# Kernel optimization log

Measured on AMD Instinct MI355X. Metric: run time of the kernel, lower is better.

## Reference

```python
import jax, jax.numpy as jnp
import numpy as np

B, T, C, H = 2, 2048, 1024, 16
HS = C // H  # head_size = 64
EPS = 1e-5


def _ln(x, g, b):
    m = jnp.mean(x, axis=-1, keepdims=True)
    v = jnp.mean(jnp.square(x - m), axis=-1, keepdims=True)
    return (x - m) * jax.lax.rsqrt(v + EPS) * g + b


def setup_inputs() -> dict:
    key = jax.random.key(0)
    ks = jax.random.split(key, 16)
    s = lambda k, shape, fan: jax.random.normal(k, shape, jnp.float32) * (fan ** -0.5)
    return {
        "x": jax.random.normal(ks[0], (B, T, C), jnp.float32),
        "Wq": s(ks[1], (H, C, HS), C), "bq": jnp.zeros((H, HS), jnp.float32),
        "Wk": s(ks[2], (H, C, HS), C), "bk": jnp.zeros((H, HS), jnp.float32),
        "Wv": s(ks[3], (H, C, HS), C), "bv": jnp.zeros((H, HS), jnp.float32),
        "Wo": s(ks[4], (C, C), C), "bo": jnp.zeros((C,), jnp.float32),
        "g1": jnp.ones((C,), jnp.float32), "b1": jnp.zeros((C,), jnp.float32),
        "g2": jnp.ones((C,), jnp.float32), "b2": jnp.zeros((C,), jnp.float32),
        "W1": s(ks[5], (C, C), C), "bf1": jnp.zeros((C,), jnp.float32),
        "W2": s(ks[6], (C, C), C), "bf2": jnp.zeros((C,), jnp.float32),
    }


def _block(x, Wq, bq, Wk, bk, Wv, bv, Wo, bo, g1, b1, g2, b2, W1, bf1, W2, bf2):
    h = _ln(x, g1, b1)
    # per-head projections, batched over heads: (B,T,C) x (H,C,HS) -> (B,H,T,HS)
    q = jnp.einsum('btc,hcd->bhtd', h, Wq) + bq[None, :, None, :]
    k = jnp.einsum('btc,hcd->bhtd', h, Wk) + bk[None, :, None, :]
    v = jnp.einsum('btc,hcd->bhtd', h, Wv) + bv[None, :, None, :]
    w = jnp.einsum('bhqd,bhkd->bhqk', q, k) * (HS ** -0.5)
    causal = jnp.tril(jnp.ones((T, T), bool))  # tril[q,k]==0 -> -inf
    w = jnp.where(causal[None, None], w, -jnp.inf)
    # FAITHFUL quirk: original uses F.softmax(w, dim=1) on (B,T,T),
    # i.e. normalization over the QUERY axis (axis=2 of bhqk).
    w = jax.nn.softmax(w, axis=2)
    att = jnp.einsum('bhqk,bhkd->bhqd', w, v)
    att = att.transpose(0, 2, 1, 3).reshape(x.shape[0], x.shape[1], -1)  # concat heads
    x = x + att @ Wo + bo
    h2 = _ln(x, g2, b2)
    x = x + jax.nn.relu(h2 @ W1 + bf1) @ W2 + bf2
    return x


def reference(x, Wq, bq, Wk, bk, Wv, bv, Wo, bo, g1, b1, g2, b2, W1, bf1, W2, bf2):
    return _block(x, Wq, bq, Wk, bk, Wv, bv, Wo, bo, g1, b1, g2, b2, W1, bf1, W2, bf2)
```

## Files before the change

### kernel.cpp

```cpp
#include <hip/hip_runtime.h>
#include <hip/hip_bf16.h>
#include <math.h>


#define B_   2
#define T_   2048
#define C_   1024
#define H_   16
#define HS_  64
#define NROWS 4096
#define C3   3072
#define K1C  0.1803368801111244f

typedef unsigned short ushort_t;
typedef __attribute__((ext_vector_type(8))) short short8;
typedef __attribute__((ext_vector_type(4))) float f32x4;
typedef __attribute__((ext_vector_type(16))) float f32x16;

__device__ __forceinline__ ushort_t f2bf(float f) {
  __hip_bfloat16 h = __float2bfloat16(f);
  ushort_t u; __builtin_memcpy(&u, &h, 2); return u;
}
__device__ __forceinline__ float bf2f(ushort_t u) {
  union { unsigned u; float f; } v; v.u = ((unsigned)u) << 16;
  return v.f;
}
__device__ __forceinline__ unsigned pkhw(float a, float b) {
  unsigned u;
  asm("v_cvt_pk_bf16_f32 %0, %1, %2" : "=v"(u) : "v"(a), "v"(b));
  return u;
}
__device__ __forceinline__ short8 mk8(unsigned a, unsigned b, unsigned c, unsigned d) {
  union { unsigned u[4]; short8 s; } t;
  t.u[0] = a; t.u[1] = b; t.u[2] = c; t.u[3] = d; return t.s;
}
__device__ __forceinline__ void pl32swap(unsigned &a, unsigned &b) {
  asm("v_permlane32_swap_b32 %0, %1" : "+v"(a), "+v"(b));
}
__device__ __forceinline__ f32x4 mfma16(short8 a, short8 b, f32x4 c) {
  return __builtin_amdgcn_mfma_f32_16x16x32_bf16(a, b, c, 0, 0, 0);
}
__device__ __forceinline__ f32x16 mfma32(short8 a, short8 b, f32x16 c) {
  return __builtin_amdgcn_mfma_f32_32x32x16_bf16(a, b, c, 0, 0, 0);
}
typedef const __attribute__((address_space(1))) void g_void;
typedef __attribute__((address_space(3))) void l_void;
__device__ __forceinline__ void gl_lds16(const void* g, void* l) {
  __builtin_amdgcn_global_load_lds((g_void*)g, (l_void*)l, 16, 0, 0);
}

__global__ __launch_bounds__(256) void ln_bf16(
    const float* __restrict__ x, const float* __restrict__ g,
    const float* __restrict__ b, ushort_t* __restrict__ out) {
  int row = blockIdx.x;
  const float* xr = x + (size_t)row * C_;
  int t = threadIdx.x;
  float4 v = ((const float4*)xr)[t];
  float s  = v.x + v.y + v.z + v.w;
  float ss = v.x*v.x + v.y*v.y + v.z*v.z + v.w*v.w;
  #pragma unroll
  for (int off = 32; off > 0; off >>= 1) {
    s  += __shfl_down(s, off);
    ss += __shfl_down(ss, off);
  }
  __shared__ float red[2][4];
  int wid = t >> 6, lane = t & 63;
  if (lane == 0) { red[0][wid] = s; red[1][wid] = ss; }
  __syncthreads();
  if (t == 0) {
    float a = 0, c = 0;
    for (int i = 0; i < 4; i++) { a += red[0][i]; c += red[1][i]; }
    red[0][0] = a; red[1][0] = c;
  }
  __syncthreads();
  float mean = red[0][0] * (1.0f / C_);
  float var  = red[1][0] * (1.0f / C_) - mean * mean;
  float r = rsqrtf(var + 1e-5f);
  float4 gv = ((const float4*)g)[t];
  float4 bv = ((const float4*)b)[t];
  ushort4 o;
  o.x = f2bf((v.x - mean) * r * gv.x + bv.x);
  o.y = f2bf((v.y - mean) * r * gv.y + bv.y);
  o.z = f2bf((v.z - mean) * r * gv.z + bv.z);
  o.w = f2bf((v.w - mean) * r * gv.w + bv.w);
  ((ushort4*)(out + (size_t)row * C_))[t] = o;
}

__global__ __launch_bounds__(256) void prep_weights(
    const float* __restrict__ Wq, const float* __restrict__ Wk,
    const float* __restrict__ Wv, const float* __restrict__ Wo,
    const float* __restrict__ W1, const float* __restrict__ W2,
    const float* __restrict__ bq, const float* __restrict__ bk,
    const float* __restrict__ bv, ushort_t* __restrict__ Wqkvt,
    ushort_t* __restrict__ Wot3, float* __restrict__ bqkv) {
  int bid = blockIdx.x;
  if (bid < 12288) {
    int idx = bid * 256 + threadIdx.x;
    int n = idx >> 10, c = idx & 1023;
    int sel = n >> 10, nn = n & 1023;
    const float* W = (sel == 0) ? Wq : ((sel == 1) ? Wk : Wv);
    Wqkvt[idx] = f2bf(W[((size_t)(nn >> 6) * C_ + c) * HS_ + (nn & 63)]);
  } else if (bid < 24576) {
    int idx = (bid - 12288) * 256 + threadIdx.x;
    int sel = idx >> 20, rem = idx & 1048575;
    int n = rem >> 10, k = rem & 1023;
    const float* W = (sel == 0) ? Wo : ((sel == 1) ? W1 : W2);
    Wot3[idx] = f2bf(W[(size_t)k * C_ + n]);
  } else {
    int i = (bid - 24576) * 256 + threadIdx.x;
    if (i < 3072)
      bqkv[i] = (i < 1024) ? bq[i] : ((i < 2048) ? bk[i - 1024] : bv[i - 2048]);
  }
}

__global__ __launch_bounds__(256) void gemm128q(
    const ushort_t* __restrict__ A, const ushort_t* __restrict__ Bt,
    const float* __restrict__ bias, ushort_t* __restrict__ Cm,
    int M, int N, int K) {
  __shared__ ushort_t As[128 * 64];
  __shared__ ushort_t Bs[128 * 64];
  int t = threadIdx.x;
  int bid = blockIdx.x;
  int xcd = bid & 7, loc = bid >> 3;
  int mb = (xcd >> 1) * 8 + (loc & 7);
  int nb = (xcd & 1) * 12 + (loc >> 3);
  int m0 = mb * 128, n0 = nb * 128;
  int w = t >> 6, l = t & 63;
  int wr = w >> 1, wc = w & 1;
  int lo = l & 15, hi = l >> 4;
  f32x4 acc[4][4] = {};
  int srow = t >> 3, ssw = (t & 7) ^ (srow & 7);
  const ushort_t* Ag = A  + (size_t)(m0 + srow) * K + ssw * 8;
  const ushort_t* Bg = Bt + (size_t)(n0 + srow) * K + ssw * 8;
  int aoff[4][2], boff[4][2];
  #pragma unroll
  for (int i = 0; i < 4; i++)
    #pragma unroll
    for (int kk = 0; kk < 2; kk++) {
      aoff[i][kk] = (wr * 64 + i * 16 + lo) * 64 + ((kk * 4 + hi) ^ (lo & 7)) * 8;
      boff[i][kk] = (wc * 64 + i * 16 + lo) * 64 + ((kk * 4 + hi) ^ (lo & 7)) * 8;
    }
  for (int k0 = 0; k0 < K; k0 += 64) {
    #pragma unroll
    for (int i = 0; i < 4; i++) {
      gl_lds16(Ag + (size_t)(i * 32) * K + k0, &As[i * 2048 + t * 8]);
      gl_lds16(Bg + (size_t)(i * 32) * K + k0, &Bs[i * 2048 + t * 8]);
    }
    __syncthreads();
    short8 af[4][2], bfr[4][2];
    #pragma unroll
    for (int i = 0; i < 4; i++)
      #pragma unroll
      for (int kk = 0; kk < 2; kk++) {
        af[i][kk]  = *(const short8*)&As[aoff[i][kk]];
        bfr[i][kk] = *(const short8*)&Bs[boff[i][kk]];
      }
    #pragma unroll
    for (int kk = 0; kk < 2; kk++)
      #pragma unroll
      for (int i = 0; i < 4; i++)
        #pragma unroll
        for (int j = 0; j < 4; j++)
          acc[i][j] = mfma16(af[i][kk], bfr[j][kk], acc[i][j]);
    __syncthreads();
  }
  float qs = (n0 < C_) ? K1C : 1.0f;
  #pragma unroll
  for (int i = 0; i < 4; i++) {
    int m = m0 + wr * 64 + i * 16 + hi * 4;
    #pragma unroll
    for (int j = 0; j < 4; j++) {
      int n = n0 + wc * 64 + j * 16 + lo;
      float bv = bias[n];
      #pragma unroll
      for (int r = 0; r < 4; r++)
        Cm[(size_t)(m + r) * N + n] = f2bf((acc[i][j][r] + bv) * qs);
    }
  }
}

template<int OUT_BF16, int RELU, int HAS_RES>
__global__ __launch_bounds__(256) void gemm64(
    const ushort_t* __restrict__ A, const ushort_t* __restrict__ Bt,
    const float* __restrict__ bias, const float* __restrict__ res,
    void* __restrict__ Cm, int M, int N, int K) {
  __shared__ ushort_t As[128 * 64];
  __shared__ ushort_t Bs[64 * 64];
  int t = threadIdx.x;
  int m0 = blockIdx.y * 128, n0 = blockIdx.x * 64;
  int w = t >> 6, l = t & 63;
  int wr = w >> 1, wc = w & 1;
  int lo = l & 15, hi = l >> 4;
  f32x4 acc[4][2] = {};
  int srow = t >> 3, ssw = (t & 7) ^ (srow & 7);
  const ushort_t* Ag = A  + (size_t)(m0 + srow) * K + ssw * 8;
  const ushort_t* Bg = Bt + (size_t)(n0 + srow) * K + ssw * 8;
  int aoff[4][2], boff[2][2];
  #pragma unroll
  for (int i = 0; i < 4; i++)
    #pragma unroll
    for (int kk = 0; kk < 2; kk++)
      aoff[i][kk] = (wr * 64 + i * 16 + lo) * 64 + ((kk * 4 + hi) ^ (lo & 7)) * 8;
  #pragma unroll
  for (int j = 0; j < 2; j++)
    #pragma unroll
    for (int kk = 0; kk < 2; kk++)
      boff[j][kk] = (wc * 32 + j * 16 + lo) * 64 + ((kk * 4 + hi) ^ (lo & 7)) * 8;
  for (int k0 = 0; k0 < K; k0 += 64) {
    #pragma unroll
    for (int i = 0; i < 4; i++)
      gl_lds16(Ag + (size_t)(i * 32) * K + k0, &As[i * 2048 + t * 8]);
    #pragma unroll
    for (int i = 0; i < 2; i++)
      gl_lds16(Bg + (size_t)(i * 32) * K + k0, &Bs[i * 2048 + t * 8]);
    __syncthreads();
    short8 af[4][2], bfr[2][2];
    #pragma unroll
    for (int i = 0; i < 4; i++)
      #pragma unroll
      for (int kk = 0; kk < 2; kk++)
        af[i][kk] = *(const short8*)&As[aoff[i][kk]];
    #pragma unroll
    for (int j = 0; j < 2; j++)
      #pragma unroll
      for (int kk = 0; kk < 2; kk++)
        bfr[j][kk] = *(const short8*)&Bs[boff[j][kk]];
    #pragma unroll
    for (int kk = 0; kk < 2; kk++)
      #pragma unroll
      for (int i = 0; i < 4; i++)
        #pragma unroll
        for (int j = 0; j < 2; j++)
          acc[i][j] = mfma16(af[i][kk], bfr[j][kk], acc[i][j]);
    __syncthreads();
  }
  #pragma unroll
  for (int i = 0; i < 4; i++) {
    int m = m0 + wr * 64 + i * 16 + hi * 4;
    #pragma unroll
    for (int j = 0; j < 2; j++) {
      int n = n0 + wc * 32 + j * 16 + lo;
      float bv = bias[n];
      #pragma unroll
      for (int r = 0; r < 4; r++) {
        float v = acc[i][j][r] + bv;
        if (HAS_RES) v += res[(size_t)(m + r) * N + n];
        if (RELU) v = fmaxf(v, 0.f);
        if (OUT_BF16) ((ushort_t*)Cm)[(size_t)(m + r) * N + n] = f2bf(v);
        else          ((float*)Cm)[(size_t)(m + r) * N + n] = v;
      }
    }
  }
}

__global__ __launch_bounds__(256) void attn_stats(
    const ushort_t* __restrict__ QKV, float* __restrict__ dinv) {
  int bid = blockIdx.x;
  int xcd = bid & 7, loc = (bid >> 3) & 31, half = bid >> 8;
  int bh = xcd * 4 + (loc & 3);
  int j = loc >> 2;
  int kb = half ? (15 - j) : j;
  int b = bh >> 4, h = bh & 15;
  int t = threadIdx.x, w = t >> 6, l = t & 63, l31 = l & 31, hi32 = l >> 5;
  __shared__ ushort_t Qs[2][4][2048];
  const ushort_t* Qb = QKV + (size_t)b * T_ * C3 + h * HS_;
  const ushort_t* Kb = Qb + C_;
  int k0w = kb * 128 + w * 32;
  short8 ka[4];
  #pragma unroll
  for (int c = 0; c < 4; c++)
    ka[c] = *(const short8*)(Kb + (size_t)(k0w + l31) * C3 + c * 16 + hi32 * 8);
  float s[16];
  #pragma unroll
  for (int r = 0; r < 16; r++) s[r] = 0.f;

  int qoff[4];
  #pragma unroll
  for (int c = 0; c < 4; c++)
    qoff[c] = l31 * 64 + ((c * 2 + hi32) ^ (l31 & 7)) * 8;

  int sr = t >> 3, slot = t & 7, su = slot ^ (sr & 7);
  const ushort_t* Qsrc = Qb + (size_t)sr * C3 + su * 8;
  int qt0 = kb * 4, cnt = 64 - qt0;
  int dqt = qt0 + w;

  #pragma unroll
  for (int sub = 0; sub < 4; sub++)
    gl_lds16(Qsrc + (size_t)(qt0 + sub) * 32 * C3, &Qs[0][sub][t * 8]);
  for (int i = 0; i < cnt; i += 4) {
    int buf = (i >> 2) & 1;
    if (i + 4 < cnt) {
      #pragma unroll
      for (int sub = 0; sub < 4; sub++)
        gl_lds16(Qsrc + (size_t)(qt0 + i + 4 + sub) * 32 * C3,
                 &Qs[buf ^ 1][sub][t * 8]);
      asm volatile("s_waitcnt vmcnt(4)");
    } else {
      asm volatile("s_waitcnt vmcnt(0)");
    }
    __builtin_amdgcn_s_barrier();
    __builtin_amdgcn_sched_barrier(0);
    #pragma unroll
    for (int sub = 0; sub < 4; sub++) {
      int qt = qt0 + i + sub;
      if (qt >= dqt) {
        const ushort_t* base = &Qs[buf][sub][0];
        short8 qf[4];
        #pragma unroll
        for (int c = 0; c < 4; c++)
          qf[c] = *(const short8*)(base + qoff[c]);
        __builtin_amdgcn_s_setprio(1);
        f32x16 d = {};
        #pragma unroll
        for (int c = 0; c < 4; c++) d = mfma32(ka[c], qf[c], d);
        __builtin_amdgcn_s_setprio(0);
        if (qt == dqt) {
          int qq = qt * 32 + l31;
          #pragma unroll
          for (int r = 0; r < 16; r++) {
            int k = k0w + (r & 3) + 8 * (r >> 2) + 4 * hi32;
            s[r] += (qq >= k) ? __builtin_amdgcn_exp2f(d[r]) : 0.f;
          }
        } else {
          #pragma unroll
          for (int r = 0; r < 16; r++) s[r] += __builtin_amdgcn_exp2f(d[r]);
        }
      }
    }
    __builtin_amdgcn_sched_barrier(0);
    __builtin_amdgcn_s_barrier();
    __builtin_amdgcn_sched_barrier(0);
  }
  #pragma unroll
  for (int off = 1; off < 32; off <<= 1)
    #pragma unroll
    for (int r = 0; r < 16; r++)
      s[r] += __shfl_xor(s[r], off);
  if (l31 == 0) {
    #pragma unroll
    for (int r = 0; r < 16; r++) {
      int k = k0w + (r & 3) + 8 * (r >> 2) + 4 * hi32;
      dinv[(size_t)bh * T_ + k] = 1.0f / s[r];
    }
  }
}

__global__ __launch_bounds__(256) void transpose_v(
    const ushort_t* __restrict__ QKV, const float* __restrict__ dinv,
    ushort_t* __restrict__ Vt) {
  int t0 = blockIdx.x * 64;
  int bh = blockIdx.y; int b = bh >> 4, h = bh & 15;
  __shared__ ushort_t tile[64][65];
  int tid = threadIdx.x;
  #pragma unroll
  for (int i = 0; i < 16; i++) {
    int idx = i * 256 + tid;
    int tt = idx >> 6, dd = idx & 63;
    float v = bf2f(QKV[(size_t)(b * T_ + t0 + tt) * C3 + 2 * C_ + h * HS_ + dd]);
    tile[tt][dd] = f2bf(v * dinv[(size_t)bh * T_ + t0 + tt]);
  }
  __syncthreads();
  #pragma unroll
  for (int i = 0; i < 16; i++) {
    int idx = i * 256 + tid;
    int dd = idx >> 6, tt = idx & 63;
    Vt[((size_t)(bh * HS_ + dd)) * T_ + t0 + tt] = tile[tt][dd];
  }
}

__global__ __launch_bounds__(256) void attn_pv(
    const ushort_t* __restrict__ QKV, const ushort_t* __restrict__ Vt,
    ushort_t* __restrict__ att) {
  int bid = blockIdx.x;
  int xcd = bid & 7, loc = (bid >> 3) & 31, half = bid >> 8;
  int bh = xcd * 4 + (loc & 3);
  int j = loc >> 2;
  int qb = half ? j : (15 - j);
  int b = bh >> 4, h = bh & 15;
  int t = threadIdx.x, w = t >> 6, l = t & 63, l31 = l & 31, hi32 = l >> 5;
  __shared__ ushort_t KV[2][4][2][2048];
  const ushort_t* Qb = QKV + (size_t)b * T_ * C3 + h * HS_;
  const ushort_t* Kb = Qb + C_;
  const ushort_t* Vb = Vt + (size_t)bh * HS_ * T_;
  int q0w = qb * 128 + w * 32;
  short8 qf[4];
  #pragma unroll
  for (int c = 0; c < 4; c++)
    qf[c] = *(const short8*)(Qb + (size_t)(q0w + l31) * C3 + c * 16 + hi32 * 8);
  f32x16 o0 = {}, o1 = {};
  int nkt = qb * 4 + 4;
  int dkt = q0w >> 5;

  int koff[4], voff[4];
  #pragma unroll
  for (int c = 0; c < 4; c++)
    koff[c] = l31 * 64 + ((c * 2 + hi32) ^ (l31 & 7)) * 8;
  #pragma unroll
  for (int i = 0; i < 4; i++) {
    int u = (i & 1) * 4 + (i >> 1) * 2 + hi32;
    voff[i] = 2048 + l31 * 64 + (u ^ (l31 & 7)) * 8;
  }

  int sr = t >> 3, slot = t & 7, su = slot ^ (sr & 7);
  int vdh = su >> 2, vc2 = su & 3;
  const ushort_t* Ksrc = Kb + (size_t)sr * C3 + su * 8;
  const ushort_t* Vsrc = Vb + (size_t)(vdh * 32 + sr) * T_ + vc2 * 8;

  #pragma unroll
  for (int sub = 0; sub < 4; sub++) {
    gl_lds16(Ksrc + (size_t)sub * 32 * C3, &KV[0][sub][0][t * 8]);
    gl_lds16(Vsrc + sub * 32,              &KV[0][sub][1][t * 8]);
  }
  for (int kt = 0; kt < nkt; kt += 4) {
    int buf = (kt >> 2) & 1;
    if (kt + 4 < nkt) {
      #pragma unroll
      for (int sub = 0; sub < 4; sub++) {
        gl_lds16(Ksrc + (size_t)(kt + 4 + sub) * 32 * C3, &KV[buf ^ 1][sub][0][t * 8]);
        gl_lds16(Vsrc + (kt + 4 + sub) * 32,              &KV[buf ^ 1][sub][1][t * 8]);
      }
      asm volatile("s_waitcnt vmcnt(8)");
    } else {
      asm volatile("s_waitcnt vmcnt(0)");
    }
    __builtin_amdgcn_s_barrier();
    __builtin_amdgcn_sched_barrier(0);
    #pragma unroll
    for (int sub = 0; sub < 4; sub++) {
      int kts = kt + sub;
      if (kts <= dkt) {
        const ushort_t* base = &KV[buf][sub][0][0];
        short8 ka[4], vf[4];
        #pragma unroll
        for (int c = 0; c < 4; c++)
          ka[c] = *(const short8*)(base + koff[c]);
        #pragma unroll
        for (int i = 0; i < 4; i++)
          vf[i] = *(const short8*)(base + voff[i]);
        __builtin_amdgcn_s_setprio(1);
        f32x16 sacc = {};
        #pragma unroll
        for (int c = 0; c < 4; c++) sacc = mfma32(ka[c], qf[c], sacc);
        __builtin_amdgcn_s_setprio(0);
        float e[16];
        if (kts == dkt) {
          int qq = q0w + l31;
          #pragma unroll
          for (int r = 0; r < 16; r++) {
            int k = kts * 32 + (r & 3) + 8 * (r >> 2) + 4 * hi32;
            e[r] = (k <= qq) ? __builtin_amdgcn_exp2f(sacc[r]) : 0.f;
          }
        } else {
          #pragma unroll
          for (int r = 0; r < 16; r++) e[r] = __builtin_amdgcn_exp2f(sacc[r]);
        }
        unsigned u[8];
        #pragma unroll
        for (int j2 = 0; j2 < 8; j2++) u[j2] = pkhw(e[2 * j2], e[2 * j2 + 1]);
        pl32swap(u[0], u[2]); pl32swap(u[1], u[3]);
        pl32swap(u[4], u[6]); pl32swap(u[5], u[7]);
        short8 pa0 = mk8(u[0], u[1], u[2], u[3]);
        short8 pa1 = mk8(u[4], u[5], u[6], u[7]);
        __builtin_amdgcn_s_setprio(1);
        o0 = mfma32(pa0, vf[0], o0);
        o1 = mfma32(pa0, vf[1], o1);
        o0 = mfma32(pa1, vf[2], o0);
        o1 = mfma32(pa1, vf[3], o1);
        __builtin_amdgcn_s_setprio(0);
      }
    }
    __builtin_amdgcn_sched_barrier(0);
    __builtin_amdgcn_s_barrier();
    __builtin_amdgcn_sched_barrier(0);
  }

  #pragma unroll
  for (int r = 0; r < 16; r++) {
    int qq = q0w + (r & 3) + 8 * (r >> 2) + 4 * hi32;
    size_t base = (size_t)(b * T_ + qq) * C_ + h * HS_;
    att[base + l31]      = f2bf(o0[r]);
    att[base + 32 + l31] = f2bf(o1[r]);
  }
}

extern "C" void kernel_launch(void* const* d_in, const int* in_sizes, int n_in,
                              void* d_out, int out_size, void* d_ws, size_t ws_size,
                              hipStream_t stream) {
  const float* x   = (const float*)d_in[0];
  const float* Wq  = (const float*)d_in[1];
  const float* bq  = (const float*)d_in[2];
  const float* Wk  = (const float*)d_in[3];
  const float* bk  = (const float*)d_in[4];
  const float* Wv  = (const float*)d_in[5];
  const float* bv  = (const float*)d_in[6];
  const float* Wo  = (const float*)d_in[7];
  const float* bo  = (const float*)d_in[8];
  const float* g1  = (const float*)d_in[9];
  const float* b1  = (const float*)d_in[10];
  const float* g2  = (const float*)d_in[11];
  const float* b2  = (const float*)d_in[12];
  const float* W1  = (const float*)d_in[13];
  const float* bf1 = (const float*)d_in[14];
  const float* W2  = (const float*)d_in[15];
  const float* bf2 = (const float*)d_in[16];
  float* out = (float*)d_out;

  char* base = (char*)d_ws;
  const size_t MB = 1 << 20;
  ushort_t* QKVb  = (ushort_t*)(base);
  ushort_t* hb    = (ushort_t*)(base + 24 * MB);
  ushort_t* Vt    = (ushort_t*)(base + 32 * MB);
  float*    y     = (float*)   (base + 40 * MB);
  ushort_t* Wqkvt = (ushort_t*)(base + 56 * MB);
  ushort_t* Wot   = (ushort_t*)(base + 62 * MB);
  ushort_t* W1t   = (ushort_t*)(base + 64 * MB);
  ushort_t* W2t   = (ushort_t*)(base + 66 * MB);
  float*    bqkv  = (float*)   (base + 68 * MB);
  float*    dinv  = (float*)   (base + 68 * MB + 65536);

  prep_weights<<<24588, 256, 0, stream>>>(Wq, Wk, Wv, Wo, W1, W2,
                                          bq, bk, bv, Wqkvt, Wot, bqkv);

  ln_bf16<<<NROWS, 256, 0, stream>>>(x, g1, b1, hb);

  gemm128q<<<768, 256, 0, stream>>>(hb, Wqkvt, bqkv, QKVb, NROWS, C3, C_);

  attn_stats<<<512, 256, 0, stream>>>(QKVb, dinv);
  transpose_v<<<dim3(T_ / 64, 32), 256, 0, stream>>>(QKVb, dinv, Vt);
  ushort_t* attb = hb;
  attn_pv<<<512, 256, 0, stream>>>(QKVb, Vt, attb);

  dim3 g64(C_ / 64, NROWS / 128);
  gemm64<0,0,1><<<g64, 256, 0, stream>>>(attb, Wot, bo, x, y, NROWS, C_, C_);

  ushort_t* h2b = QKVb;
  ln_bf16<<<NROWS, 256, 0, stream>>>(y, g2, b2, h2b);
  ushort_t* f1b = Vt;
  gemm64<1,1,0><<<g64, 256, 0, stream>>>(h2b, W1t, bf1, nullptr, f1b, NROWS, C_, C_);
  gemm64<0,0,1><<<g64, 256, 0, stream>>>(f1b, W2t, bf2, y, out, NROWS, C_, C_);
}
```

Before: 204.4 us.

## Double-buffer LDS in both GEMM kernels with BK=32 and async prefetch

Both GEMM kernels now use two LDS buffers with K-tiles of 32 instead of one buffer with K-tiles of 64. The next tile's global-to-LDS loads are issued before computing on the current tile, using explicit vmcnt waits and raw barriers, so load latency can overlap with MFMA work. The LDS swizzle is redone for 32-wide rows, and the MFMA section is wrapped in s_setprio. Halving BK doubles the barrier count per unit of work and leaves a shallow prefetch depth.

```diff
diff --git a/kernel.cpp b/kernel.cpp
--- a/kernel.cpp
+++ b/kernel.cpp
@@ -117,8 +117,8 @@
     const ushort_t* __restrict__ A, const ushort_t* __restrict__ Bt,
     const float* __restrict__ bias, ushort_t* __restrict__ Cm,
     int M, int N, int K) {
-  __shared__ ushort_t As[128 * 64];
-  __shared__ ushort_t Bs[128 * 64];
+  __shared__ ushort_t As[2][128 * 32];
+  __shared__ ushort_t Bs[2][128 * 32];
   int t = threadIdx.x;
   int bid = blockIdx.x;
   int xcd = bid & 7, loc = bid >> 3;
@@ -129,40 +129,52 @@
   int wr = w >> 1, wc = w & 1;
   int lo = l & 15, hi = l >> 4;
   f32x4 acc[4][4] = {};
-  int srow = t >> 3, ssw = (t & 7) ^ (srow & 7);
-  const ushort_t* Ag = A  + (size_t)(m0 + srow) * K + ssw * 8;
-  const ushort_t* Bg = Bt + (size_t)(n0 + srow) * K + ssw * 8;
-  int aoff[4][2], boff[4][2];
-  #pragma unroll
-  for (int i = 0; i < 4; i++)
-    #pragma unroll
-    for (int kk = 0; kk < 2; kk++) {
-      aoff[i][kk] = (wr * 64 + i * 16 + lo) * 64 + ((kk * 4 + hi) ^ (lo & 7)) * 8;
-      boff[i][kk] = (wc * 64 + i * 16 + lo) * 64 + ((kk * 4 + hi) ^ (lo & 7)) * 8;
-    }
-  for (int k0 = 0; k0 < K; k0 += 64) {
+  int srow = t >> 2;
+  int sslot = (t & 3) ^ ((srow >> 1) & 3);
+  const ushort_t* Ag = A  + (size_t)(m0 + srow) * K + sslot * 8;
+  const ushort_t* Bg = Bt + (size_t)(n0 + srow) * K + sslot * 8;
+  int key = (lo >> 1) & 3;
+  int aoff[4], boff[4];
+  #pragma unroll
+  for (int i = 0; i < 4; i++) {
+    aoff[i] = (wr * 64 + i * 16 + lo) * 32 + (hi ^ key) * 8;
+    boff[i] = (wc * 64 + i * 16 + lo) * 32 + (hi ^ key) * 8;
+  }
+  int nkt = K >> 5;
+  gl_lds16(Ag,          &As[0][t * 8]);
+  gl_lds16(Ag + 64 * K, &As[0][64 * 32 + t * 8]);
+  gl_lds16(Bg,          &Bs[0][t * 8]);
+  gl_lds16(Bg + 64 * K, &Bs[0][64 * 32 + t * 8]);
+  for (int kt = 0; kt < nkt; kt++) {
+    int cur = kt & 1;
+    if (kt + 1 < nkt) {
+      int k0 = (kt + 1) * 32;
+      gl_lds16(Ag + k0,          &As[cur ^ 1][t * 8]);
+      gl_lds16(Ag + 64 * K + k0, &As[cur ^ 1][64 * 32 + t * 8]);
+      gl_lds16(Bg + k0,          &Bs[cur ^ 1][t * 8]);
+      gl_lds16(Bg + 64 * K + k0, &Bs[cur ^ 1][64 * 32 + t * 8]);
+      asm volatile("s_waitcnt vmcnt(4)");
+    } else {
+      asm volatile("s_waitcnt vmcnt(0)");
+    }
+    __builtin_amdgcn_s_barrier();
+    __builtin_amdgcn_sched_barrier(0);
+    short8 af[4], bfr[4];
     #pragma unroll
     for (int i = 0; i < 4; i++) {
-      gl_lds16(Ag + (size_t)(i * 32) * K + k0, &As[i * 2048 + t * 8]);
-      gl_lds16(Bg + (size_t)(i * 32) * K + k0, &Bs[i * 2048 + t * 8]);
-    }
-    __syncthreads();
-    short8 af[4][2], bfr[4][2];
+      af[i]  = *(const short8*)&As[cur][aoff[i]];
+      bfr[i] = *(const short8*)&Bs[cur][boff[i]];
+    }
+    __builtin_amdgcn_s_setprio(1);
     #pragma unroll
     for (int i = 0; i < 4; i++)
       #pragma unroll
-      for (int kk = 0; kk < 2; kk++) {
-        af[i][kk]  = *(const short8*)&As[aoff[i][kk]];
-        bfr[i][kk] = *(const short8*)&Bs[boff[i][kk]];
-      }
-    #pragma unroll
-    for (int kk = 0; kk < 2; kk++)
-      #pragma unroll
-      for (int i = 0; i < 4; i++)
-        #pragma unroll
-        for (int j = 0; j < 4; j++)
-          acc[i][j] = mfma16(af[i][kk], bfr[j][kk], acc[i][j]);
-    __syncthreads();
+      for (int j = 0; j < 4; j++)
+        acc[i][j] = mfma16(af[i], bfr[j], acc[i][j]);
+    __builtin_amdgcn_s_setprio(0);
+    __builtin_amdgcn_sched_barrier(0);
+    __builtin_amdgcn_s_barrier();
+    __builtin_amdgcn_sched_barrier(0);
   }
   float qs = (n0 < C_) ? K1C : 1.0f;
   #pragma unroll
@@ -184,55 +196,60 @@
     const ushort_t* __restrict__ A, const ushort_t* __restrict__ Bt,
     const float* __restrict__ bias, const float* __restrict__ res,
     void* __restrict__ Cm, int M, int N, int K) {
-  __shared__ ushort_t As[128 * 64];
-  __shared__ ushort_t Bs[64 * 64];
+  __shared__ ushort_t As[2][128 * 32];
+  __shared__ ushort_t Bs[2][64 * 32];
   int t = threadIdx.x;
   int m0 = blockIdx.y * 128, n0 = blockIdx.x * 64;
   int w = t >> 6, l = t & 63;
   int wr = w >> 1, wc = w & 1;
   int lo = l & 15, hi = l >> 4;
   f32x4 acc[4][2] = {};
-  int srow = t >> 3, ssw = (t & 7) ^ (srow & 7);
-  const ushort_t* Ag = A  + (size_t)(m0 + srow) * K + ssw * 8;
-  const ushort_t* Bg = Bt + (size_t)(n0 + srow) * K + ssw * 8;
-  int aoff[4][2], boff[2][2];
+  int srow = t >> 2;
+  int sslot = (t & 3) ^ ((srow >> 1) & 3);
+  const ushort_t* Ag = A  + (size_t)(m0 + srow) * K + sslot * 8;
+  const ushort_t* Bg = Bt + (size_t)(n0 + srow) * K + sslot * 8;
+  int key = (lo >> 1) & 3;
+  int aoff[4], boff[2];
   #pragma unroll
   for (int i = 0; i < 4; i++)
-    #pragma unroll
-    for (int kk = 0; kk < 2; kk++)
-      aoff[i][kk] = (wr * 64 + i * 16 + lo) * 64 + ((kk * 4 + hi) ^ (lo & 7)) * 8;
+    aoff[i] = (wr * 64 + i * 16 + lo) * 32 + (hi ^ key) * 8;
   #pragma unroll
   for (int j = 0; j < 2; j++)
-    #pragma unroll
-    for (int kk = 0; kk < 2; kk++)
-      boff[j][kk] = (wc * 32 + j * 16 + lo) * 64 + ((kk * 4 + hi) ^ (lo & 7)) * 8;
-  for (int k0 = 0; k0 < K; k0 += 64) {
+    boff[j] = (wc * 32 + j * 16 + lo) * 32 + (hi ^ key) * 8;
+  int nkt = K >> 5;
+  gl_lds16(Ag,          &As[0][t * 8]);
+  gl_lds16(Ag + 64 * K, &As[0][64 * 32 + t * 8]);
+  gl_lds16(Bg,          &Bs[0][t * 8]);
+  for (int kt = 0; kt < nkt; kt++) {
+    int cur = kt & 1;
+    if (kt + 1 < nkt) {
+      int k0 = (kt + 1) * 32;
+      gl_lds16(Ag + k0,          &As[cur ^ 1][t * 8]);
+      gl_lds16(Ag + 64 * K + k0, &As[cur ^ 1][64 * 32 + t * 8]);
+      gl_lds16(Bg + k0,          &Bs[cur ^ 1][t * 8]);
+      asm volatile("s_waitcnt vmcnt(3)");
+    } else {
+      asm volatile("s_waitcnt vmcnt(0)");
+    }
+    __builtin_amdgcn_s_barrier();
+    __builtin_amdgcn_sched_barrier(0);
+    short8 af[4], bfr[2];
     #pragma unroll
     for (int i = 0; i < 4; i++)
-      gl_lds16(Ag + (size_t)(i * 32) * K + k0, &As[i * 2048 + t * 8]);
-    #pragma unroll
-    for (int i = 0; i < 2; i++)
-      gl_lds16(Bg + (size_t)(i * 32) * K + k0, &Bs[i * 2048 + t * 8]);
-    __syncthreads();
-    short8 af[4][2], bfr[2][2];
+      af[i] = *(const short8*)&As[cur][aoff[i]];
+    #pragma unroll
+    for (int j = 0; j < 2; j++)
+      bfr[j] = *(const short8*)&Bs[cur][boff[j]];
+    __builtin_amdgcn_s_setprio(1);
     #pragma unroll
     for (int i = 0; i < 4; i++)
       #pragma unroll
-      for (int kk = 0; kk < 2; kk++)
-        af[i][kk] = *(const short8*)&As[aoff[i][kk]];
-    #pragma unroll
-    for (int j = 0; j < 2; j++)
-      #pragma unroll
-      for (int kk = 0; kk < 2; kk++)
-        bfr[j][kk] = *(const short8*)&Bs[boff[j][kk]];
-    #pragma unroll
-    for (int kk = 0; kk < 2; kk++)
-      #pragma unroll
-      for (int i = 0; i < 4; i++)
-        #pragma unroll
-        for (int j = 0; j < 2; j++)
-          acc[i][j] = mfma16(af[i][kk], bfr[j][kk], acc[i][j]);
-    __syncthreads();
+      for (int j = 0; j < 2; j++)
+        acc[i][j] = mfma16(af[i], bfr[j], acc[i][j]);
+    __builtin_amdgcn_s_setprio(0);
+    __builtin_amdgcn_sched_barrier(0);
+    __builtin_amdgcn_s_barrier();
+    __builtin_amdgcn_sched_barrier(0);
   }
   #pragma unroll
   for (int i = 0; i < 4; i++) {
```

Measured after the change: 202.5 us. Within noise of the previous version (-0.9%).
